# Performance work log

Measured on AMD Instinct MI355X. Metric: run time of the kernel, lower is better.

Reference implementation:

```python
import math
import jax, jax.numpy as jnp
import numpy as np

N_ORDERS = 2
CHUNK = 64  # tokens per chunk (before virtual-token expansion)


def _expand_derivative(x, n):
    """expand_virtual_tokens(mode='derivative'): [B,H,S,D] -> [B,H,S*n,D]."""
    B, H, S, D = x.shape
    pad = jnp.zeros((B, H, n - 1, D), x.dtype)
    xp = jnp.concatenate([pad, x], axis=2)  # [B,H,S+n-1,D]
    coeffs = np.array([(-1) ** kk * math.comb(n - 1, kk) for kk in range(n)], dtype=np.float32)
    coeffs = coeffs / np.abs(coeffs).sum()  # L1-normalized binomial coeffs
    # window j at token t is x_pad[t+j]*coeffs[j]; then flip window dim (as in torch .flip(-1))
    win = jnp.stack([xp[:, :, j:j + S, :] * coeffs[j] for j in range(n)], axis=3)  # [B,H,S,n,D]
    win = win[:, :, :, ::-1, :]
    return win.reshape(B, H, S * n, D)


def _unlinear(x, scale=2.0):
    """unlinear_activation: gated norm-scaled gelu applied to inter-chunk state."""
    xn = jnp.linalg.norm(x, axis=-1, keepdims=True) + 1e-6
    return x / scale * jax.nn.gelu(scale * x / xn, approximate=True)


def _stab(x):
    # ensure_stability: clamp to [-1e4, 1e4], nan -> center (0)
    return jnp.nan_to_num(jnp.clip(x, -1e4, 1e4), nan=0.0, posinf=1e4, neginf=-1e4)


def _forward(q, k, v, beta):
    n = N_ORDERS
    B, H, S, D = q.shape
    qe = _expand_derivative(q, n)
    ke = _expand_derivative(k, n)
    ve = _expand_derivative(v, n)
    be = jnp.repeat(beta, n, axis=-1)[..., None]  # [B,H,S*n,1]
    w = ke * be  # delta-rule write keys
    u = ve * be  # delta-rule write values

    Cn = CHUNK * n                     # virtual tokens per chunk
    NC = (S * n) // Cn                 # number of chunks
    ch = lambda x: x.reshape(B, H, NC, Cn, D)
    qc, kc, wc, uc = ch(qe), ch(ke), ch(w), ch(u)

    # triangular (forward-substitution) inversion per chunk:
    # T = (I + tril(W K^T, -1))^{-1}  == fast_invert_matrix of the strictly-lower system
    A = jnp.tril(jnp.einsum('bhnid,bhnjd->bhnij', wc, kc), -1)
    eye = jnp.eye(Cn, dtype=q.dtype)
    T = jax.scipy.linalg.solve_triangular(
        eye + A, jnp.broadcast_to(eye, A.shape), lower=True, unit_diagonal=True)
    wci = jnp.einsum('bhnij,bhnjd->bhnid', T, wc)
    uci = jnp.einsum('bhnij,bhnjd->bhnid', T, uc)

    def chunk_step(h, xs):
        # sequential_delta_product_scan body: per-token Householder updates, n_orders steps
        qx, wx, ux = xs  # each [B,H,Cn,D]
        C = CHUNK
        qr = qx.reshape(B, H, C, n, D)
        wr = wx.reshape(B, H, C, n, D)
        ur = ux.reshape(B, H, C, n, D)
        state = jnp.broadcast_to(h[:, :, None], (B, H, C, D, D))  # per-token state
        outs = []
        for s in range(n):
            qs, ws, us = qr[:, :, :, s], wr[:, :, :, s], ur[:, :, :, s]
            kho = jnp.einsum('bhcd,bhcde->bhce', ws, state)
            uval = us - kho
            o_inter = jnp.einsum('bhcd,bhcde->bhce', qs, state)
            o_intra = qs * uval
            state = _stab(state + jnp.einsum('bhcd,bhce->bhcde', ws, uval))
            outs.append(o_intra + o_inter)
        o = jnp.stack(outs, axis=3).reshape(B, H, C * n, D)  # interleave: pos t*n+s
        h_new = _unlinear(state[:, :, -1])  # linear_activation=False path
        return h_new, o

    xs = (jnp.moveaxis(qc, 2, 0), jnp.moveaxis(wci, 2, 0), jnp.moveaxis(uci, 2, 0))
    h0 = jnp.zeros((B, H, D, D), q.dtype)
    _, os = jax.lax.scan(chunk_step, h0, xs)  # os: [NC,B,H,Cn,D]
    out_v = jnp.moveaxis(os, 0, 2).reshape(B, H, S, n, D)
    return out_v[..., n - 1, :]  # collapse virtual tokens: keep last-order output per token


def setup_inputs() -> dict:
    key = jax.random.key(0)
    kq, kk, kv, kb = jax.random.split(key, 4)
    B, H, S, D = 2, 16, 2048, 64
    return {
        'q': jax.random.normal(kq, (B, H, S, D), jnp.float32),
        'k': jax.random.normal(kk, (B, H, S, D), jnp.float32),
        'v': jax.random.normal(kv, (B, H, S, D), jnp.float32),
        'beta': jax.random.uniform(kb, (B, H, S), jnp.float32),
    }


def reference(q, k, v, beta):
    return _forward(q, k, v, beta)
```

## Files before the change

### kernel.cpp

```cpp
#include <hip/hip_runtime.h>
#include <math.h>


namespace {
constexpr int PAIRS = 32;
constexpr int SLEN  = 2048;
constexpr int D     = 64;
constexpr int CK    = 64;
constexpr int CN    = 128;
constexpr int NCH   = 32;
constexpr int NB2   = 16;
constexpr int NP    = 5;

__device__ __forceinline__ float stab1(float x) {
    float y = __builtin_amdgcn_fmed3f(x, -10000.f, 10000.f);
    return (x != x) ? 0.f : y;
}

__device__ __forceinline__ int kidx(int a, int f4) {
    return a * 68 + 4 * (f4 ^ ((a >> 2) & 3));
}
}

__global__ __launch_bounds__(512, 1)
void la_phase1(const float* __restrict__ kg, const float* __restrict__ vg,
               const float* __restrict__ bg, float* __restrict__ ws)
{
    __shared__ float Ysh[CN][CN];
    __shared__ float Gm[65][66];
    __shared__ char  ureg[36864];
    __shared__ float bq4[CK], bh[CK];

    float* kstf = (float*)ureg;
    float* scm  = (float*)ureg;
    float (*redsh)[3][8][CN] = (float(*)[3][8][CN])(ureg + 12288);

    const int blk  = blockIdx.x;
    const int p    = blk >> 5;
    const int nc   = blk & 31;
    const int tid  = threadIdx.x;
    const int baseT = nc * CK;
    const float* kp = kg + (size_t)p * SLEN * D;
    const float* vp = vg + (size_t)p * SLEN * D;
    const float* bp = bg + (size_t)p * SLEN;

    for (int u = tid; u < 65 * 16; u += 512) {
        int a = u >> 4, f4 = u & 15;
        int src = baseT - 1 + a;
        float4 val = float4{0.f, 0.f, 0.f, 0.f};
        if (src >= 0) val = ((const float4*)(kp + (size_t)src * D))[f4];
        *(float4*)&kstf[kidx(a, f4)] = val;
    }
    if (tid < CK) {
        float bv = bp[baseT + tid];
        bq4[tid] = 0.25f * bv;
        bh[tid]  = 0.5f  * bv;
    }
    __syncthreads();

    for (int u = tid; u < CN * 32; u += 512) {
        int i = u >> 5, f4i = u & 31;
        int ci = i >> 1, si = i & 1;
        float sc = si ? bh[ci] : -bh[ci];
        float4 val = float4{0.f, 0.f, 0.f, 0.f};
        if (f4i < 16) {
            val = *(const float4*)&kstf[kidx(ci - si + 1, f4i)];
        } else {
            int srcT = baseT + ci - si;
            if (srcT >= 0) val = ((const float4*)(vp + (size_t)srcT * D))[f4i - 16];
        }
        val.x *= sc; val.y *= sc; val.z *= sc; val.w *= sc;
        *(float4*)&Ysh[i][f4i * 4] = val;
    }

    for (int tt = tid; tt < 17 * 17; tt += 512) {
        int ta = tt / 17, tb = tt % 17;
        if (tb > ta) continue;
        int a0 = ta * 4, b0 = tb * 4;
        float acc[4][4] = {};
        for (int d4 = 0; d4 < 16; ++d4) {
            float4 av[4], bv[4];
            #pragma unroll
            for (int r = 0; r < 4; ++r) {
                av[r] = *(const float4*)&kstf[kidx(min(a0 + r, 64), d4)];
                bv[r] = *(const float4*)&kstf[kidx(min(b0 + r, 64), d4)];
            }
            #pragma unroll
            for (int r = 0; r < 4; ++r)
                #pragma unroll
                for (int c = 0; c < 4; ++c)
                    acc[r][c] += av[r].x * bv[c].x + av[r].y * bv[c].y
                               + av[r].z * bv[c].z + av[r].w * bv[c].w;
        }
        #pragma unroll
        for (int r = 0; r < 4; ++r)
            #pragma unroll
            for (int c = 0; c < 4; ++c)
                if (a0 + r <= 64 && b0 + c <= 64) {
                    Gm[a0 + r][b0 + c] = acc[r][c];
                    Gm[b0 + c][a0 + r] = acc[r][c];
                }
    }
    __syncthreads();

    for (int e = tid; e < 192; e += 512) {
        int gp = (e < 64) ? 0 : 1;
        int ee = e - gp * 64;
        int j = ee >> 3, r = ee & 7;
        int i = 8 * gp + r;
        int ai = (i >> 1) - (i & 1) + 1;
        int aj = (j >> 1) - (j & 1) + 1;
        float sgn = ((i ^ j) & 1) ? -1.f : 1.f;
        scm[(gp * CN + j) * 8 + r] = sgn * bq4[i >> 1] * Gm[ai][aj];
    }
    __syncthreads();

    const int col = tid & 127;
    const int grp = tid >> 7;

    for (int g = 0; g < 16; ++g) {
        const int bufG  = g % 3;
        const int bufG1 = (g + 1) % 3;
        const int bufG2 = (g + 2) % 3;

        if (grp == 0) {
            float acc[8] = {};
            if (g > 0) {
                #pragma unroll
                for (int r = 0; r < 8; ++r)
                    acc[r] = redsh[g & 1][0][r][col] + redsh[g & 1][1][r][col]
                           + redsh[g & 1][2][r][col];
                #pragma unroll
                for (int jj = 0; jj < 8; ++jj) {
                    int j = 8 * g - 8 + jj;
                    float yv = Ysh[j][col];
                    const float4 a03 = *(const float4*)&scm[(bufG * CN + j) * 8];
                    const float4 a47 = *(const float4*)&scm[(bufG * CN + j) * 8 + 4];
                    acc[0] += a03.x * yv; acc[1] += a03.y * yv;
                    acc[2] += a03.z * yv; acc[3] += a03.w * yv;
                    acc[4] += a47.x * yv; acc[5] += a47.y * yv;
                    acc[6] += a47.z * yv; acc[7] += a47.w * yv;
                }
            }
            float yn[8];
            #pragma unroll
            for (int r = 0; r < 8; ++r) {
                float val = Ysh[8 * g + r][col] - acc[r];
                #pragma unroll
                for (int rp = 0; rp < 8; ++rp)
                    if (rp < r) val -= scm[(bufG * CN + 8 * g + rp) * 8 + r] * yn[rp];
                yn[r] = val;
                Ysh[8 * g + r][col] = val;
            }
        } else {
            if (g + 2 <= 15) {
                int gb = g + 2, jmax = 8 * gb + 8;
                for (int e = tid - 128; e < 8 * jmax; e += 384) {
                    int j = e >> 3, r = e & 7;
                    int i = 8 * gb + r;
                    int ai = (i >> 1) - (i & 1) + 1;
                    int aj = (j >> 1) - (j & 1) + 1;
                    float sgn = ((i ^ j) & 1) ? -1.f : 1.f;
                    scm[(bufG2 * CN + j) * 8 + r] = sgn * bq4[i >> 1] * Gm[ai][aj];
                }
            }
            if (g + 1 <= 15) {
                float acc[8] = {};
                for (int j = grp - 1; j < 8 * g; j += 3) {
                    float yv = Ysh[j][col];
                    const float4 a03 = *(const float4*)&scm[(bufG1 * CN + j) * 8];
                    const float4 a47 = *(const float4*)&scm[(bufG1 * CN + j) * 8 + 4];
                    acc[0] += a03.x * yv; acc[1] += a03.y * yv;
                    acc[2] += a03.z * yv; acc[3] += a03.w * yv;
                    acc[4] += a47.x * yv; acc[5] += a47.y * yv;
                    acc[6] += a47.z * yv; acc[7] += a47.w * yv;
                }
                #pragma unroll
                for (int r = 0; r < 8; ++r)
                    redsh[(g + 1) & 1][grp - 1][r][col] = acc[r];
            }
        }
        __syncthreads();
    }

    float* gY = ws + (size_t)(p * NCH + nc) * (CN * CN);
    for (int u = tid; u < CN * 32; u += 512) {
        int r = u >> 5, f4 = u & 31;
        *(float4*)&gY[r * CN + f4 * 4] = *(const float4*)&Ysh[r][f4 * 4];
    }
}

__global__ __launch_bounds__(512, 4)
void la_phase2(const float* __restrict__ qg, const float* __restrict__ ws,
               float* __restrict__ outg)
{
    __shared__ float WU[2][NP][256];
    __shared__ float Qs[2][NP][64];
    __shared__ float pR1[8][NP][64];
    __shared__ float pKH[8][NP][64];
    __shared__ float pOA[8][NP][64];

    const int blk  = blockIdx.x;
    const int p    = blk >> 4, nb = blk & 15;
    const int tid  = threadIdx.x;
    const int w    = tid >> 6, lane = tid & 63;

    const float* qp = qg + (size_t)p * SLEN * D;
    float* op = outg + (size_t)p * SLEN * D;
    const float* wsbase = ws + (size_t)p * NCH * (CN * CN);

    const int cMain = nb * 4 + w;

    float4 wuR = float4{0.f, 0.f, 0.f, 0.f};
    float  qR  = 0.f;

    auto stage_load = [&](int nc) {
        const float* gY = wsbase + (size_t)nc * (CN * CN);
        if (w < 4) {
            wuR = *(const float4*)(gY + (size_t)(2 * cMain) * CN + lane * 4);
            int t = nc * CK + cMain;
            qR = qp[(size_t)((t > 0) ? t - 1 : 0) * D + lane];
        } else if (w == 4) {
            wuR = *(const float4*)(gY + (size_t)126 * CN + lane * 4);
            qR = qp[(size_t)(nc * CK + 62) * D + lane];
        }
    };
    auto stage_write = [&](int buf) {
        if (w < NP) {
            *(float4*)&WU[buf][w][lane * 4] = wuR;
            Qs[buf][w][lane] = qR;
        }
    };

    float hs[8];
    #pragma unroll
    for (int j = 0; j < 8; ++j) hs[j] = 0.f;

    stage_load(0);
    stage_write(0);
    __syncthreads();

    for (int nc = 0; nc < NCH; ++nc) {
        const int buf = nc & 1;
        if (nc + 1 < NCH) stage_load(nc + 1);

        #pragma unroll
        for (int P = 0; P < NP; ++P) {
            float4 a = *(const float4*)&WU[buf][P][8 * w];
            float4 b = *(const float4*)&WU[buf][P][8 * w + 4];
            pR1[w][P][lane] =
                  ((a.x * hs[0] + a.y * hs[1]) + (a.z * hs[2] + a.w * hs[3]))
                + ((b.x * hs[4] + b.y * hs[5]) + (b.z * hs[6] + b.w * hs[7]));
        }
        __syncthreads();

        float uv0r[NP];
        #pragma unroll
        for (int P = 0; P < NP; ++P) {
            float s = 0.f;
            #pragma unroll
            for (int wv = 0; wv < 8; ++wv) s += pR1[wv][P][lane];
            uv0r[P] = WU[buf][P][64 + lane] - s;
        }

        #pragma unroll
        for (int P = 0; P < NP; ++P) {
            float uv0 = uv0r[P];
            float4 w0a = *(const float4*)&WU[buf][P][8 * w];
            float4 w0b = *(const float4*)&WU[buf][P][8 * w + 4];
            float4 w1a = *(const float4*)&WU[buf][P][128 + 8 * w];
            float4 w1b = *(const float4*)&WU[buf][P][128 + 8 * w + 4];
            float4 qa  = *(const float4*)&Qs[buf][P][8 * w];
            float4 qb  = *(const float4*)&Qs[buf][P][8 * w + 4];
            float st0 = stab1(hs[0] + w0a.x * uv0);
            float st1 = stab1(hs[1] + w0a.y * uv0);
            float st2 = stab1(hs[2] + w0a.z * uv0);
            float st3 = stab1(hs[3] + w0a.w * uv0);
            float st4 = stab1(hs[4] + w0b.x * uv0);
            float st5 = stab1(hs[5] + w0b.y * uv0);
            float st6 = stab1(hs[6] + w0b.z * uv0);
            float st7 = stab1(hs[7] + w0b.w * uv0);
            pKH[w][P][lane] =
                  ((w1a.x * st0 + w1a.y * st1) + (w1a.z * st2 + w1a.w * st3))
                + ((w1b.x * st4 + w1b.y * st5) + (w1b.z * st6 + w1b.w * st7));
            pOA[w][P][lane] =
                  ((qa.x * st0 + qa.y * st1) + (qa.z * st2 + qa.w * st3))
                + ((qb.x * st4 + qb.y * st5) + (qb.z * st6 + qb.w * st7));
        }
        stage_write(buf ^ 1);
        __syncthreads();

        if (w < 4) {
            float skh = 0.f, soa = 0.f;
            #pragma unroll
            for (int wv = 0; wv < 8; ++wv) {
                skh += pKH[wv][w][lane];
                soa += pOA[wv][w][lane];
            }
            float uv1 = WU[buf][w][192 + lane] - skh;
            int t = nc * CK + cMain;
            float outv = 0.5f * (Qs[buf][w][lane] * uv1 + soa);
            op[(size_t)t * D + lane] = (t > 0) ? outv : 0.f;
        }

        float skh4 = 0.f;
        #pragma unroll
        for (int wv = 0; wv < 8; ++wv) skh4 += pKH[wv][4][lane];
        const float uv1l = WU[buf][4][192 + lane] - skh4;
        const float uv0l = uv0r[4];

        {
            float4 w0a = *(const float4*)&WU[buf][4][8 * w];
            float4 w0b = *(const float4*)&WU[buf][4][8 * w + 4];
            float4 w1a = *(const float4*)&WU[buf][4][128 + 8 * w];
            float4 w1b = *(const float4*)&WU[buf][4][128 + 8 * w + 4];
            float st2v[8], ss[8];
            st2v[0] = stab1(stab1(hs[0] + w0a.x * uv0l) + w1a.x * uv1l);
            st2v[1] = stab1(stab1(hs[1] + w0a.y * uv0l) + w1a.y * uv1l);
            st2v[2] = stab1(stab1(hs[2] + w0a.z * uv0l) + w1a.z * uv1l);
            st2v[3] = stab1(stab1(hs[3] + w0a.w * uv0l) + w1a.w * uv1l);
            st2v[4] = stab1(stab1(hs[4] + w0b.x * uv0l) + w1b.x * uv1l);
            st2v[5] = stab1(stab1(hs[5] + w0b.y * uv0l) + w1b.y * uv1l);
            st2v[6] = stab1(stab1(hs[6] + w0b.z * uv0l) + w1b.z * uv1l);
            st2v[7] = stab1(stab1(hs[7] + w0b.w * uv0l) + w1b.w * uv1l);
            #pragma unroll
            for (int j = 0; j < 8; ++j) ss[j] = st2v[j] * st2v[j];
            #pragma unroll
            for (int msk = 1; msk < 64; msk <<= 1) {
                #pragma unroll
                for (int j = 0; j < 8; ++j) ss[j] += __shfl_xor(ss[j], msk);
            }
            #pragma unroll
            for (int j = 0; j < 8; ++j) {
                float xn = __builtin_amdgcn_sqrtf(ss[j]) + 1e-6f;
                float y  = 2.f * st2v[j] * __builtin_amdgcn_rcpf(xn);
                float y2 = y * y;
                float e  = __builtin_amdgcn_exp2f(y * (2.3022078f + 0.1029432f * y2));
                float th = (e - 1.f) * __builtin_amdgcn_rcpf(e + 1.f);
                hs[j] = 0.25f * st2v[j] * y * (1.f + th);
            }
        }
    }
}

extern "C" void kernel_launch(void* const* d_in, const int* in_sizes, int n_in,
                              void* d_out, int out_size, void* d_ws, size_t ws_size,
                              hipStream_t stream)
{
    (void)in_sizes; (void)n_in; (void)out_size; (void)ws_size;
    const float* q    = (const float*)d_in[0];
    const float* k    = (const float*)d_in[1];
    const float* v    = (const float*)d_in[2];
    const float* beta = (const float*)d_in[3];
    float* ws  = (float*)d_ws;
    float* out = (float*)d_out;

    la_phase1<<<PAIRS * NCH, 512, 0, stream>>>(k, v, beta, ws);
    la_phase2<<<PAIRS * NB2, 512, 0, stream>>>(q, ws, out);
}
```

Measured before the change: 322.9 us.

## Move recurrent state to shared memory and row-partition the norm/gelu update

The per-chunk state moves from registers (each thread holding 8 rows of one column) into a padded shared-memory array. The end-of-chunk norm and gelu update is re-partitioned so each group of 8 threads owns one state row, which turns the 6-step, 8-value wave-wide butterfly into a 3-step shuffle on a single value. In exchange it adds two extra block barriers per chunk, shared-memory round trips to reload the state, and about 17 KB more LDS, which may lower occupancy.

```diff
diff --git a/kernel.cpp b/kernel.cpp
--- a/kernel.cpp
+++ b/kernel.cpp
@@ -199,11 +199,16 @@
     __shared__ float pR1[8][NP][64];
     __shared__ float pKH[8][NP][64];
     __shared__ float pOA[8][NP][64];
+    __shared__ float UV0[NP][64];
+    __shared__ float UV1r[64];
+    __shared__ float hsh[64][67];
 
     const int blk  = blockIdx.x;
     const int p    = blk >> 4, nb = blk & 15;
     const int tid  = threadIdx.x;
     const int w    = tid >> 6, lane = tid & 63;
+    const int hd   = tid >> 3;
+    const int he0  = (tid & 7) * 8;
 
     const float* qp = qg + (size_t)p * SLEN * D;
     float* op = outg + (size_t)p * SLEN * D;
@@ -232,16 +237,18 @@
         }
     };
 
-    float hs[8];
-    #pragma unroll
-    for (int j = 0; j < 8; ++j) hs[j] = 0.f;
-
+    for (int idx = tid; idx < 64 * 67; idx += 512) (&hsh[0][0])[idx] = 0.f;
     stage_load(0);
     stage_write(0);
     __syncthreads();
 
     for (int nc = 0; nc < NCH; ++nc) {
         const int buf = nc & 1;
+
+        float hs[8];
+        #pragma unroll
+        for (int j = 0; j < 8; ++j) hs[j] = hsh[8 * w + j][lane];
+
         if (nc + 1 < NCH) stage_load(nc + 1);
 
         #pragma unroll
@@ -254,18 +261,17 @@
         }
         __syncthreads();
 
-        float uv0r[NP];
+        if (w < NP) {
+            float s = 0.f;
+            #pragma unroll
+            for (int wv = 0; wv < 8; ++wv) s += pR1[wv][w][lane];
+            UV0[w][lane] = WU[buf][w][64 + lane] - s;
+        }
+        __syncthreads();
+
         #pragma unroll
         for (int P = 0; P < NP; ++P) {
-            float s = 0.f;
-            #pragma unroll
-            for (int wv = 0; wv < 8; ++wv) s += pR1[wv][P][lane];
-            uv0r[P] = WU[buf][P][64 + lane] - s;
-        }
-
-        #pragma unroll
-        for (int P = 0; P < NP; ++P) {
-            float uv0 = uv0r[P];
+            float uv0 = UV0[P][lane];
             float4 w0a = *(const float4*)&WU[buf][P][8 * w];
             float4 w0b = *(const float4*)&WU[buf][P][8 * w + 4];
             float4 w1a = *(const float4*)&WU[buf][P][128 + 8 * w];
@@ -301,45 +307,42 @@
             int t = nc * CK + cMain;
             float outv = 0.5f * (Qs[buf][w][lane] * uv1 + soa);
             op[(size_t)t * D + lane] = (t > 0) ? outv : 0.f;
-        }
-
-        float skh4 = 0.f;
-        #pragma unroll
-        for (int wv = 0; wv < 8; ++wv) skh4 += pKH[wv][4][lane];
-        const float uv1l = WU[buf][4][192 + lane] - skh4;
-        const float uv0l = uv0r[4];
+        } else if (w == 4) {
+            float skh = 0.f;
+            #pragma unroll
+            for (int wv = 0; wv < 8; ++wv) skh += pKH[wv][4][lane];
+            UV1r[lane] = WU[buf][4][192 + lane] - skh;
+        }
+        __syncthreads();
 
         {
-            float4 w0a = *(const float4*)&WU[buf][4][8 * w];
-            float4 w0b = *(const float4*)&WU[buf][4][8 * w + 4];
-            float4 w1a = *(const float4*)&WU[buf][4][128 + 8 * w];
-            float4 w1b = *(const float4*)&WU[buf][4][128 + 8 * w + 4];
-            float st2v[8], ss[8];
-            st2v[0] = stab1(stab1(hs[0] + w0a.x * uv0l) + w1a.x * uv1l);
-            st2v[1] = stab1(stab1(hs[1] + w0a.y * uv0l) + w1a.y * uv1l);
-            st2v[2] = stab1(stab1(hs[2] + w0a.z * uv0l) + w1a.z * uv1l);
-            st2v[3] = stab1(stab1(hs[3] + w0a.w * uv0l) + w1a.w * uv1l);
-            st2v[4] = stab1(stab1(hs[4] + w0b.x * uv0l) + w1b.x * uv1l);
-            st2v[5] = stab1(stab1(hs[5] + w0b.y * uv0l) + w1b.y * uv1l);
-            st2v[6] = stab1(stab1(hs[6] + w0b.z * uv0l) + w1b.z * uv1l);
-            st2v[7] = stab1(stab1(hs[7] + w0b.w * uv0l) + w1b.w * uv1l);
-            #pragma unroll
-            for (int j = 0; j < 8; ++j) ss[j] = st2v[j] * st2v[j];
-            #pragma unroll
-            for (int msk = 1; msk < 64; msk <<= 1) {
-                #pragma unroll
-                for (int j = 0; j < 8; ++j) ss[j] += __shfl_xor(ss[j], msk);
-            }
+            float w0d = WU[buf][4][hd];
+            float w1d = WU[buf][4][128 + hd];
+            float st2v[8];
+            float ssum = 0.f;
             #pragma unroll
             for (int j = 0; j < 8; ++j) {
-                float xn = __builtin_amdgcn_sqrtf(ss[j]) + 1e-6f;
-                float y  = 2.f * st2v[j] * __builtin_amdgcn_rcpf(xn);
+                float st1 = stab1(hsh[hd][he0 + j] + w0d * UV0[4][he0 + j]);
+                float st2 = stab1(st1 + w1d * UV1r[he0 + j]);
+                st2v[j] = st2;
+                ssum += st2 * st2;
+            }
+            ssum += __shfl_xor(ssum, 1);
+            ssum += __shfl_xor(ssum, 2);
+            ssum += __shfl_xor(ssum, 4);
+            float xn = __builtin_amdgcn_sqrtf(ssum) + 1e-6f;
+            float s2 = 2.f * __builtin_amdgcn_rcpf(xn);
+            #pragma unroll
+            for (int j = 0; j < 8; ++j) {
+                float x  = st2v[j];
+                float y  = x * s2;
                 float y2 = y * y;
                 float e  = __builtin_amdgcn_exp2f(y * (2.3022078f + 0.1029432f * y2));
                 float th = (e - 1.f) * __builtin_amdgcn_rcpf(e + 1.f);
-                hs[j] = 0.25f * st2v[j] * y * (1.f + th);
-            }
-        }
+                hsh[hd][he0 + j] = 0.25f * x * y * (1.f + th);
+            }
+        }
+        __syncthreads();
     }
 }
 
```

Measured after the change: 275.1 us. -14.8%, faster.
